# Kernel tuning notes

Hardware: AMD Instinct MI355X
Metric: run time of the kernel (lower is better)

The kernel has to match this reference:

```python
import jax, jax.numpy as jnp
import numpy as np

N = 50000
E = 600000
D_IN = 128
D_HID = 128
D_OUT = 40
EPS = 1e-5


def glorot(key, shape):
    lim = float(np.sqrt(6.0 / (shape[0] + shape[1])))
    return jax.random.uniform(key, shape, jnp.float32, -lim, lim)


def setup_inputs() -> dict:
    key = jax.random.key(0)
    ks = jax.random.split(key, 8)
    return {
        "node_feat": jax.random.normal(ks[0], (N, D_IN), jnp.float32),
        "edge_src": jax.random.randint(ks[1], (E,), 0, N, jnp.int32),
        "edge_dst": jax.random.randint(ks[2], (E,), 0, N, jnp.int32),
        # input BatchNorm (bn_1)
        "bn0_g": jnp.ones((D_IN,), jnp.float32),
        "bn0_b": jnp.zeros((D_IN,), jnp.float32),
        # conv 1 (in -> hidden) + its BN
        "W1": glorot(ks[3], (D_IN, D_HID)),
        "b1": jnp.zeros((D_HID,), jnp.float32),
        "bn1_g": jnp.ones((D_HID,), jnp.float32),
        "bn1_b": jnp.zeros((D_HID,), jnp.float32),
        # conv 2 (hidden -> hidden) + its BN
        "W2": glorot(ks[4], (D_HID, D_HID)),
        "b2": jnp.zeros((D_HID,), jnp.float32),
        "bn2_g": jnp.ones((D_HID,), jnp.float32),
        "bn2_b": jnp.zeros((D_HID,), jnp.float32),
        # final projection
        "Wf": glorot(ks[5], (D_HID, D_OUT)),
        "bf": jnp.zeros((D_OUT,), jnp.float32),
    }


def batchnorm(x, gamma, beta):
    # BatchNorm1d over nodes (batch-stat / training-mode normalization)
    mu = jnp.mean(x, axis=0)
    var = jnp.mean(jnp.square(x - mu), axis=0)
    return gamma * (x - mu) * jax.lax.rsqrt(var + EPS) + beta


def gcn_conv(x, W, b, src, dst, norm, self_norm):
    # GCNConv: D^{-1/2}(A+I)D^{-1/2} X W + b
    h = x @ W  # [N, d_out]
    agg = jax.ops.segment_sum(h[src] * norm[:, None], dst, num_segments=N)
    agg = agg + h * self_norm[:, None]  # self-loop contribution
    return agg + b


def reference(node_feat, edge_src, edge_dst, bn0_g, bn0_b, W1, b1, bn1_g, bn1_b,
              W2, b2, bn2_g, bn2_b, Wf, bf):
    # degree with self-loops: deg_i = |{e : dst(e)=i}| + 1
    deg = jnp.ones((N,), jnp.float32).at[edge_dst].add(1.0)
    dinv = jax.lax.rsqrt(deg)
    norm = dinv[edge_src] * dinv[edge_dst]  # [E]
    self_norm = dinv * dinv                 # [N]

    x = batchnorm(node_feat, bn0_g, bn0_b)

    x = gcn_conv(x, W1, b1, edge_src, edge_dst, norm, self_norm)
    x = batchnorm(x, bn1_g, bn1_b)
    x = jax.nn.relu(x)  # dropout is identity in eval mode

    x = gcn_conv(x, W2, b2, edge_src, edge_dst, norm, self_norm)
    x = batchnorm(x, bn2_g, bn2_b)
    x = jax.nn.relu(x)

    return x @ Wf + bf  # [N, D_OUT]
```

## Files before the change

kernel.cpp:

```cpp
#include <hip/hip_runtime.h>
#include <cstdint>
#include <cstddef>


#define CS_BLOCKS 512

typedef short s8v __attribute__((ext_vector_type(8)));
typedef float f4v __attribute__((ext_vector_type(4)));

__device__ inline ushort f2bf(float f) {
    uint u = __float_as_uint(f);
    return (ushort)((u + 0x7fffu + ((u >> 16) & 1u)) >> 16);
}
__device__ inline float2 bf2f2(uint u) {
    float2 r;
    r.x = __uint_as_float(u << 16);
    r.y = __uint_as_float(u & 0xffff0000u);
    return r;
}

__global__ __launch_bounds__(256) void k_prolog(const float* __restrict__ X,
                                                int n, float* __restrict__ part,
                                                const float* __restrict__ W1,
                                                const float* __restrict__ W2,
                                                ushort* __restrict__ Wswz,
                                                int* __restrict__ cnt) {
    const int bid = blockIdx.x;
    if (bid < CS_BLOCKS) {
        __shared__ float ls[8 * 128];
        __shared__ float lq[8 * 128];
        const int c4    = threadIdx.x & 31;
        const int rslot = threadIdx.x >> 5;
        float4 s4 = make_float4(0.f, 0.f, 0.f, 0.f);
        float4 q4 = make_float4(0.f, 0.f, 0.f, 0.f);
        const float4* X4 = (const float4*)X;
        for (int r = bid * 8 + rslot; r < n; r += CS_BLOCKS * 8) {
            float4 v = X4[(size_t)r * 32 + c4];
            s4.x += v.x; s4.y += v.y; s4.z += v.z; s4.w += v.w;
            q4.x = fmaf(v.x, v.x, q4.x); q4.y = fmaf(v.y, v.y, q4.y);
            q4.z = fmaf(v.z, v.z, q4.z); q4.w = fmaf(v.w, v.w, q4.w);
        }
        *(float4*)&ls[rslot * 128 + c4 * 4] = s4;
        *(float4*)&lq[rslot * 128 + c4 * 4] = q4;
        __syncthreads();
        float t = 0.f;
        if (threadIdx.x < 128) {
            int c = threadIdx.x;
            #pragma unroll
            for (int k = 0; k < 8; ++k) t += ls[k * 128 + c];
        } else {
            int c = threadIdx.x - 128;
            #pragma unroll
            for (int k = 0; k < 8; ++k) t += lq[k * 128 + c];
        }
        part[bid * 256 + threadIdx.x] = t;
    } else if (bid < CS_BLOCKS + 16) {
        const int wb = bid - CS_BLOCKS;
        const float* W = (wb < 8) ? W1 : W2;
        ushort* out = Wswz + (wb < 8 ? 0 : 16384);
        int t  = (wb & 7) * 256 + threadIdx.x;
        int l  = t & 63;
        int fi = t >> 6;
        int ks = fi & 3, ct = fi >> 2;
        int c  = ct * 16 + (l & 15);
        int k0 = ks * 32 + ((l >> 4) << 3);
        ushort o[8];
        #pragma unroll
        for (int j = 0; j < 8; ++j)
            o[j] = f2bf(W[(size_t)(k0 + j) * 128 + c]);
        ushort4* dst = (ushort4*)(out + (size_t)t * 8);
        dst[0] = make_ushort4(o[0], o[1], o[2], o[3]);
        dst[1] = make_ushort4(o[4], o[5], o[6], o[7]);
    } else {
        const int zb = bid - CS_BLOCKS - 16;
        const int nv = n >> 2;
        int4* c4p = (int4*)cnt;
        const int4 z = make_int4(0, 0, 0, 0);
        for (int i = zb * 256 + threadIdx.x; i < nv; i += 64 * 256)
            c4p[i] = z;
        int i = (nv << 2) + zb * 256 + threadIdx.x;
        if (i < n) cnt[i] = 0;
    }
}

__global__ __launch_bounds__(256) void k_redA(const float* __restrict__ part,
                                              float* __restrict__ part2,
                                              int nrows) {
    const int c = threadIdx.x;
    const int b = blockIdx.x;
    const int per = (nrows + 63) >> 6;
    const int r0 = b * per;
    const int r1 = min(r0 + per, nrows);
    float t0 = 0.f, t1 = 0.f;
    int r = r0;
    for (; r + 2 <= r1; r += 2) {
        t0 += part[(size_t)r * 256 + c];
        t1 += part[(size_t)(r + 1) * 256 + c];
    }
    if (r < r1) t0 += part[(size_t)r * 256 + c];
    part2[b * 256 + c] = t0 + t1;
}

__global__ __launch_bounds__(1024) void k_bnfinal(const float* __restrict__ part,
                                                  int nrows,
                                                  const float* __restrict__ g,
                                                  const float* __restrict__ be,
                                                  float invn,
                                                  float* __restrict__ a,
                                                  float* __restrict__ b) {
    __shared__ float sh[4][256];
    const int c = threadIdx.x & 255;
    const int q = threadIdx.x >> 8;
    const int per = nrows >> 2;
    float t = 0.f;
    for (int r = q * per; r < q * per + per; r += 4) {
        t += part[(r + 0) * 256 + c] + part[(r + 1) * 256 + c]
           + part[(r + 2) * 256 + c] + part[(r + 3) * 256 + c];
    }
    sh[q][c] = t;
    __syncthreads();
    if (threadIdx.x < 128) {
        int cc = threadIdx.x;
        float su = sh[0][cc] + sh[1][cc] + sh[2][cc] + sh[3][cc];
        float sq = sh[0][cc + 128] + sh[1][cc + 128]
                 + sh[2][cc + 128] + sh[3][cc + 128];
        float mu  = su * invn;
        float var = sq * invn - mu * mu;
        float av  = g[cc] * rsqrtf(var + 1e-5f);
        a[cc] = av;
        b[cc] = be[cc] - mu * av;
    }
}

__global__ __launch_bounds__(256) void k_count(const int* __restrict__ dst, int e,
                                               int* __restrict__ cnt,
                                               int* __restrict__ rank) {
    int i = blockIdx.x * 256 + threadIdx.x;
    if (i < e) rank[i] = atomicAdd(&cnt[dst[i]], 1);
}

__global__ __launch_bounds__(1024) void k_scanA(const int* __restrict__ cnt, int n,
                                                int* __restrict__ rs, int* __restrict__ bsum) {
    __shared__ int tmp[1024];
    int t = threadIdx.x;
    int i = blockIdx.x * 1024 + t;
    int v = (i < n) ? cnt[i] : 0;
    tmp[t] = v;
    __syncthreads();
    for (int off = 1; off < 1024; off <<= 1) {
        int x = (t >= off) ? tmp[t - off] : 0;
        __syncthreads();
        tmp[t] += x;
        __syncthreads();
    }
    if (i < n) rs[i] = tmp[t] - v;
    if (t == 1023) bsum[blockIdx.x] = tmp[t];
}

__global__ __launch_bounds__(256) void k_scanC(int* __restrict__ rs,
                                               const int* __restrict__ bsum,
                                               const int* __restrict__ cnt,
                                               float* __restrict__ dinv,
                                               int n, int e) {
    __shared__ int base;
    int chunk = (int)(blockIdx.x >> 2);
    if (threadIdx.x == 0) {
        int s = 0;
        for (int c = 0; c < chunk; ++c) s += bsum[c];
        base = s;
    }
    __syncthreads();
    int i = blockIdx.x * 256 + threadIdx.x;
    if (i < n) {
        rs[i] += base;
        dinv[i] = rsqrtf((float)(cnt[i] + 1));
    }
    if (blockIdx.x == 0 && threadIdx.x == 0) rs[n] = e;
}

__global__ __launch_bounds__(256) void k_fill(const int* __restrict__ src,
                                              const int* __restrict__ dst, int e,
                                              const int* __restrict__ rs,
                                              const int* __restrict__ rank,
                                              const float* __restrict__ dinv,
                                              int2* __restrict__ ep) {
    int i = blockIdx.x * 256 + threadIdx.x;
    if (i < e) {
        int d = dst[i], s = src[i];
        int p = rs[d] + rank[i];
        float nm = dinv[s] * dinv[d];
        ep[p] = make_int2(s, __float_as_int(nm));
    }
}

__global__ __launch_bounds__(256) void k_gemm_mfma(const float* __restrict__ X,
                                                   const ushort* __restrict__ Wswz,
                                                   const float* __restrict__ av,
                                                   const float* __restrict__ bv,
                                                   int relu,
                                                   ushort* __restrict__ H, int n) {
    __shared__ ushort xb[64 * 128];
    const int tid  = threadIdx.x;
    const int row0 = blockIdx.x * 64;

    for (int i = tid; i < 64 * 32; i += 256) {
        int r = i >> 5, c4 = i & 31;
        int gr = row0 + r;
        float4 v = make_float4(0.f, 0.f, 0.f, 0.f);
        if (gr < n) v = ((const float4*)X)[(size_t)gr * 32 + c4];
        float4 a4 = ((const float4*)av)[c4];
        float4 b4 = ((const float4*)bv)[c4];
        v.x = fmaf(v.x, a4.x, b4.x);
        v.y = fmaf(v.y, a4.y, b4.y);
        v.z = fmaf(v.z, a4.z, b4.z);
        v.w = fmaf(v.w, a4.w, b4.w);
        if (relu) {
            v.x = fmaxf(v.x, 0.f); v.y = fmaxf(v.y, 0.f);
            v.z = fmaxf(v.z, 0.f); v.w = fmaxf(v.w, 0.f);
        }
        ushort4 pk = make_ushort4(f2bf(v.x), f2bf(v.y), f2bf(v.z), f2bf(v.w));
        int off = (r * 256 + c4 * 8) ^ ((r & 7) << 4);
        *(ushort4*)((char*)xb + off) = pk;
    }
    __syncthreads();

    const int wv = tid >> 6;
    const int l  = tid & 63;
    const int arow = wv * 16 + (l & 15);

    s8v afr[4];
    #pragma unroll
    for (int ks = 0; ks < 4; ++ks) {
        int off = (arow * 256 + ks * 64 + ((l >> 4) << 4)) ^ ((arow & 7) << 4);
        afr[ks] = *(const s8v*)((const char*)xb + off);
    }

    const s8v* wf = (const s8v*)Wswz;
    f4v acc[8];
    #pragma unroll
    for (int ct = 0; ct < 8; ++ct) {
        f4v c = {0.f, 0.f, 0.f, 0.f};
        #pragma unroll
        for (int ks = 0; ks < 4; ++ks) {
            s8v bb = wf[(ct * 4 + ks) * 64 + l];
            c = __builtin_amdgcn_mfma_f32_16x16x32_bf16(afr[ks], bb, c, 0, 0, 0);
        }
        acc[ct] = c;
    }

    const int rbase = row0 + wv * 16 + ((l >> 4) << 2);
    const int cidx  = l & 15;
    #pragma unroll
    for (int r = 0; r < 4; ++r) {
        int gr = rbase + r;
        if (gr < n) {
            #pragma unroll
            for (int ct = 0; ct < 8; ++ct)
                H[(size_t)gr * 128 + ct * 16 + cidx] = f2bf(acc[ct][r]);
        }
    }
}

template<int NP>
__device__ inline void pair_batch(const ushort* __restrict__ H,
                                  const int2* __restrict__ ep,
                                  int i, int half, int sl,
                                  float& a0, float& a1, float& a2, float& a3) {
    int2 p[NP]; uint2 v[NP];
    #pragma unroll
    for (int k = 0; k < NP; ++k) p[k] = ep[i + 2 * k + half];
    #pragma unroll
    for (int k = 0; k < NP; ++k)
        v[k] = ((const uint2*)(H + (size_t)p[k].x * 128))[sl];
    #pragma unroll
    for (int k = 0; k < NP; ++k) {
        float w = __int_as_float(p[k].y);
        float2 f0 = bf2f2(v[k].x);
        float2 f1 = bf2f2(v[k].y);
        a0 = fmaf(w, f0.x, a0); a1 = fmaf(w, f0.y, a1);
        a2 = fmaf(w, f1.x, a2); a3 = fmaf(w, f1.y, a3);
    }
}

__global__ __launch_bounds__(256) void k_aggregate(const ushort* __restrict__ H,
                                                   const int* __restrict__ rs,
                                                   const int2* __restrict__ ep,
                                                   const float* __restrict__ dinv,
                                                   float* __restrict__ AGG,
                                                   float* __restrict__ part, int n) {
    __shared__ float red[4][128];
    __shared__ float redq[4][128];
    const int wv   = threadIdx.x >> 6;
    const int lane = threadIdx.x & 63;
    const int half = lane >> 5;
    const int sl   = lane & 31;
    const int node = blockIdx.x * 4 + wv;
    float a0 = 0.f, a1 = 0.f, a2 = 0.f, a3 = 0.f;

    if (node < n) {
        if (half == 0) {
            float sn = dinv[node]; sn *= sn;
            uint2 sv = ((const uint2*)(H + (size_t)node * 128))[sl];
            float2 f0 = bf2f2(sv.x), f1 = bf2f2(sv.y);
            a0 = sn * f0.x; a1 = sn * f0.y;
            a2 = sn * f1.x; a3 = sn * f1.y;
        }
        int i  = rs[node];
        int i1 = rs[node + 1];
        for (; i + 16 <= i1; i += 16) pair_batch<8>(H, ep, i, half, sl, a0, a1, a2, a3);
        if (i + 8 <= i1) { pair_batch<4>(H, ep, i, half, sl, a0, a1, a2, a3); i += 8; }
        if (i + 4 <= i1) { pair_batch<2>(H, ep, i, half, sl, a0, a1, a2, a3); i += 4; }
        if (i + 2 <= i1) { pair_batch<1>(H, ep, i, half, sl, a0, a1, a2, a3); i += 2; }
        if (i < i1) {
            int2 p = ep[i];
            float w = (half == 0) ? __int_as_float(p.y) : 0.f;
            uint2 v = ((const uint2*)(H + (size_t)p.x * 128))[sl];
            float2 f0 = bf2f2(v.x), f1 = bf2f2(v.y);
            a0 = fmaf(w, f0.x, a0); a1 = fmaf(w, f0.y, a1);
            a2 = fmaf(w, f1.x, a2); a3 = fmaf(w, f1.y, a3);
        }
        a0 += __shfl_xor(a0, 32);
        a1 += __shfl_xor(a1, 32);
        a2 += __shfl_xor(a2, 32);
        a3 += __shfl_xor(a3, 32);
        if (half == 0)
            ((float4*)(AGG + (size_t)node * 128))[sl] =
                make_float4(a0, a1, a2, a3);
    }

    if (half == 0) {
        *(float4*)&red[wv][4 * sl]  = make_float4(a0, a1, a2, a3);
        *(float4*)&redq[wv][4 * sl] = make_float4(a0 * a0, a1 * a1,
                                                  a2 * a2, a3 * a3);
    }
    __syncthreads();
    const int t = threadIdx.x;
    if (t < 128)
        part[(size_t)blockIdx.x * 256 + t] =
            red[0][t] + red[1][t] + red[2][t] + red[3][t];
    else {
        int c = t - 128;
        part[(size_t)blockIdx.x * 256 + t] =
            redq[0][c] + redq[1][c] + redq[2][c] + redq[3][c];
    }
}

__global__ __launch_bounds__(256) void k_gemm_out(const float* __restrict__ X,
                                                  const float* __restrict__ Wf,
                                                  const float* __restrict__ bfv,
                                                  const float* __restrict__ a,
                                                  const float* __restrict__ b,
                                                  float* __restrict__ OUT, int n) {
    __shared__ float xl[32 * 132];
    __shared__ float wt[40 * 132];
    const int tid = threadIdx.x;

    for (int i = tid; i < 128 * 40; i += 256) {
        int c = i / 40;
        int j = i - c * 40;
        wt[j * 132 + c] = Wf[i];
    }
    const int row0 = blockIdx.x * 32;
    for (int i = tid; i < 32 * 32; i += 256) {
        int r = i >> 5, c4 = i & 31;
        int gr = row0 + r;
        float4 v = make_float4(0.f, 0.f, 0.f, 0.f);
        if (gr < n) v = ((const float4*)X)[(size_t)gr * 32 + c4];
        float4 a4 = ((const float4*)a)[c4];
        float4 b4 = ((const float4*)b)[c4];
        v.x = fmaxf(fmaf(v.x, a4.x, b4.x), 0.f);
        v.y = fmaxf(fmaf(v.y, a4.y, b4.y), 0.f);
        v.z = fmaxf(fmaf(v.z, a4.z, b4.z), 0.f);
        v.w = fmaxf(fmaf(v.w, a4.w, b4.w), 0.f);
        *(float4*)&xl[r * 132 + (c4 << 2)] = v;
    }
    __syncthreads();

    const int rg = tid >> 3;
    const int cg = tid & 7;
    const int j0 = cg * 5;
    float acc[5] = {0.f, 0.f, 0.f, 0.f, 0.f};
    for (int c = 0; c < 128; c += 4) {
        float4 xv = *(const float4*)&xl[rg * 132 + c];
        #pragma unroll
        for (int j = 0; j < 5; ++j) {
            float4 wv = *(const float4*)&wt[(j0 + j) * 132 + c];
            acc[j] = fmaf(xv.x, wv.x, acc[j]);
            acc[j] = fmaf(xv.y, wv.y, acc[j]);
            acc[j] = fmaf(xv.z, wv.z, acc[j]);
            acc[j] = fmaf(xv.w, wv.w, acc[j]);
        }
    }
    int gr = row0 + rg;
    if (gr < n) {
        #pragma unroll
        for (int j = 0; j < 5; ++j)
            OUT[(size_t)gr * 40 + j0 + j] = acc[j] + bfv[j0 + j];
    }
}

extern "C" void kernel_launch(void* const* d_in, const int* in_sizes, int n_in,
                              void* d_out, int out_size, void* d_ws, size_t ws_size,
                              hipStream_t stream) {
    const float* X0      = (const float*)d_in[0];
    const int*   edgesrc = (const int*)d_in[1];
    const int*   edgedst = (const int*)d_in[2];
    const float* bn0g = (const float*)d_in[3];
    const float* bn0b = (const float*)d_in[4];
    const float* W1   = (const float*)d_in[5];
    const float* bn1g = (const float*)d_in[7];
    const float* bn1b = (const float*)d_in[8];
    const float* W2   = (const float*)d_in[9];
    const float* bn2g = (const float*)d_in[11];
    const float* bn2b = (const float*)d_in[12];
    const float* Wf   = (const float*)d_in[13];
    const float* bfv  = (const float*)d_in[14];

    const int n = in_sizes[0] / 128;
    const int e = in_sizes[1];
    float* OUT = (float*)d_out;

    const int aggBlocks = (n + 3) / 4;

    ushort* H    = (ushort*)d_ws;
    float*  AGG  = (float*)(H + (size_t)n * 128);
    float*  dinv = AGG + (size_t)n * 128;
    int2*   ep   = (int2*)(dinv + n);
    ushort* Wswz = (ushort*)(ep + e);
    int*    cnt  = (int*)(Wswz + 2 * 16384);
    int*    rs   = cnt + n;
    int*    rank = rs + n + 1;
    int*    bsum = rank + e;
    float*  part = (float*)(bsum + 64);
    float* part2 = part + (size_t)aggBlocks * 256;
    float* a0 = part2 + 64 * 256;       float* b0 = a0 + 128;
    float* a1 = b0 + 128;               float* b1 = a1 + 128;
    float* a2 = b1 + 128;               float* b2 = a2 + 128;

    const float invn = 1.f / (float)n;
    const int nb = (n + 1023) / 1024;

    k_prolog<<<CS_BLOCKS + 16 + 64, 256, 0, stream>>>(X0, n, part, W1, W2,
                                                      Wswz, cnt);

    k_count<<<(e + 255) / 256, 256, 0, stream>>>(edgedst, e, cnt, rank);
    k_scanA<<<nb, 1024, 0, stream>>>(cnt, n, rs, bsum);
    k_scanC<<<(n + 255) / 256, 256, 0, stream>>>(rs, bsum, cnt, dinv, n, e);
    k_fill<<<(e + 255) / 256, 256, 0, stream>>>(edgesrc, edgedst, e, rs, rank,
                                                dinv, ep);

    const int gemmBlocks = (n + 63) / 64;

    k_bnfinal<<<1, 1024, 0, stream>>>(part, CS_BLOCKS, bn0g, bn0b, invn, a0, b0);
    k_gemm_mfma<<<gemmBlocks, 256, 0, stream>>>(X0, Wswz, a0, b0, 0, H, n);
    k_aggregate<<<aggBlocks, 256, 0, stream>>>(H, rs, ep, dinv, AGG, part, n);

    k_redA<<<64, 256, 0, stream>>>(part, part2, aggBlocks);
    k_bnfinal<<<1, 1024, 0, stream>>>(part2, 64, bn1g, bn1b, invn, a1, b1);
    k_gemm_mfma<<<gemmBlocks, 256, 0, stream>>>(AGG, Wswz + 16384, a1, b1, 1, H, n);
    k_aggregate<<<aggBlocks, 256, 0, stream>>>(H, rs, ep, dinv, AGG, part, n);

    k_redA<<<64, 256, 0, stream>>>(part, part2, aggBlocks);
    k_bnfinal<<<1, 1024, 0, stream>>>(part2, 64, bn2g, bn2b, invn, a2, b2);
    k_gemm_out<<<(n + 31) / 32, 256, 0, stream>>>(AGG, Wf, bfv, a2, b2, OUT, n);
}
```

Measured before the change: 244.5 us.

## Fuse BN finalize into GEMM prologues and widen aggregate gathers to 16 bytes

Drops the single-block k_bnfinal launches. Each GEMM block now reduces the 64-row partial sums itself and computes the BN scale and shift in shared memory, which removes three serialized tiny kernels at the cost of redundant per-block reduction work. The aggregation kernel switches from two half-wave edge streams with 8-byte loads to four quarter-wave streams with 16-byte bf16 loads, combined by two shuffle stages. This raises memory-level parallelism per node for the gather.

```diff
diff --git a/kernel.cpp b/kernel.cpp
--- a/kernel.cpp
+++ b/kernel.cpp
@@ -101,35 +101,26 @@
     part2[b * 256 + c] = t0 + t1;
 }
 
-__global__ __launch_bounds__(1024) void k_bnfinal(const float* __restrict__ part,
-                                                  int nrows,
-                                                  const float* __restrict__ g,
-                                                  const float* __restrict__ be,
-                                                  float invn,
-                                                  float* __restrict__ a,
-                                                  float* __restrict__ b) {
-    __shared__ float sh[4][256];
-    const int c = threadIdx.x & 255;
-    const int q = threadIdx.x >> 8;
-    const int per = nrows >> 2;
+__device__ inline void bn_inblock(const float* __restrict__ part2,
+                                  const float* __restrict__ g,
+                                  const float* __restrict__ be,
+                                  float invn, float* __restrict__ tmp,
+                                  float* __restrict__ abuf,
+                                  float* __restrict__ bbuf) {
+    const int tid = threadIdx.x;
     float t = 0.f;
-    for (int r = q * per; r < q * per + per; r += 4) {
-        t += part[(r + 0) * 256 + c] + part[(r + 1) * 256 + c]
-           + part[(r + 2) * 256 + c] + part[(r + 3) * 256 + c];
-    }
-    sh[q][c] = t;
-    __syncthreads();
-    if (threadIdx.x < 128) {
-        int cc = threadIdx.x;
-        float su = sh[0][cc] + sh[1][cc] + sh[2][cc] + sh[3][cc];
-        float sq = sh[0][cc + 128] + sh[1][cc + 128]
-                 + sh[2][cc + 128] + sh[3][cc + 128];
-        float mu  = su * invn;
-        float var = sq * invn - mu * mu;
-        float av  = g[cc] * rsqrtf(var + 1e-5f);
-        a[cc] = av;
-        b[cc] = be[cc] - mu * av;
-    }
+    #pragma unroll 8
+    for (int r = 0; r < 64; ++r) t += part2[r * 256 + tid];
+    tmp[tid] = t;
+    __syncthreads();
+    if (tid < 128) {
+        float mu  = tmp[tid] * invn;
+        float var = tmp[tid + 128] * invn - mu * mu;
+        float av  = g[tid] * rsqrtf(var + 1e-5f);
+        abuf[tid] = av;
+        bbuf[tid] = be[tid] - mu * av;
+    }
+    __syncthreads();
 }
 
 __global__ __launch_bounds__(256) void k_count(const int* __restrict__ dst, int e,
@@ -195,21 +186,26 @@
 
 __global__ __launch_bounds__(256) void k_gemm_mfma(const float* __restrict__ X,
                                                    const ushort* __restrict__ Wswz,
-                                                   const float* __restrict__ av,
-                                                   const float* __restrict__ bv,
-                                                   int relu,
+                                                   const float* __restrict__ part2,
+                                                   const float* __restrict__ g,
+                                                   const float* __restrict__ be,
+                                                   float invn, int relu,
                                                    ushort* __restrict__ H, int n) {
     __shared__ ushort xb[64 * 128];
+    __shared__ float tmp[256];
+    __shared__ float abuf[128], bbuf[128];
     const int tid  = threadIdx.x;
     const int row0 = blockIdx.x * 64;
+
+    bn_inblock(part2, g, be, invn, tmp, abuf, bbuf);
 
     for (int i = tid; i < 64 * 32; i += 256) {
         int r = i >> 5, c4 = i & 31;
         int gr = row0 + r;
         float4 v = make_float4(0.f, 0.f, 0.f, 0.f);
         if (gr < n) v = ((const float4*)X)[(size_t)gr * 32 + c4];
-        float4 a4 = ((const float4*)av)[c4];
-        float4 b4 = ((const float4*)bv)[c4];
+        float4 a4 = *(const float4*)&abuf[c4 * 4];
+        float4 b4 = *(const float4*)&bbuf[c4 * 4];
         v.x = fmaf(v.x, a4.x, b4.x);
         v.y = fmaf(v.y, a4.y, b4.y);
         v.z = fmaf(v.z, a4.z, b4.z);
@@ -262,23 +258,24 @@
 }
 
 template<int NP>
-__device__ inline void pair_batch(const ushort* __restrict__ H,
+__device__ inline void quad_batch(const ushort* __restrict__ H,
                                   const int2* __restrict__ ep,
-                                  int i, int half, int sl,
-                                  float& a0, float& a1, float& a2, float& a3) {
-    int2 p[NP]; uint2 v[NP];
-    #pragma unroll
-    for (int k = 0; k < NP; ++k) p[k] = ep[i + 2 * k + half];
+                                  int i, int q, int sl, float* __restrict__ a) {
+    int2 p[NP]; uint4 v[NP];
+    #pragma unroll
+    for (int k = 0; k < NP; ++k) p[k] = ep[i + 4 * k + q];
     #pragma unroll
     for (int k = 0; k < NP; ++k)
-        v[k] = ((const uint2*)(H + (size_t)p[k].x * 128))[sl];
+        v[k] = ((const uint4*)(H + (size_t)p[k].x * 128))[sl];
     #pragma unroll
     for (int k = 0; k < NP; ++k) {
         float w = __int_as_float(p[k].y);
-        float2 f0 = bf2f2(v[k].x);
-        float2 f1 = bf2f2(v[k].y);
-        a0 = fmaf(w, f0.x, a0); a1 = fmaf(w, f0.y, a1);
-        a2 = fmaf(w, f1.x, a2); a3 = fmaf(w, f1.y, a3);
+        float2 f0 = bf2f2(v[k].x), f1 = bf2f2(v[k].y);
+        float2 f2 = bf2f2(v[k].z), f3 = bf2f2(v[k].w);
+        a[0] = fmaf(w, f0.x, a[0]); a[1] = fmaf(w, f0.y, a[1]);
+        a[2] = fmaf(w, f1.x, a[2]); a[3] = fmaf(w, f1.y, a[3]);
+        a[4] = fmaf(w, f2.x, a[4]); a[5] = fmaf(w, f2.y, a[5]);
+        a[6] = fmaf(w, f3.x, a[6]); a[7] = fmaf(w, f3.y, a[7]);
     }
 }
 
@@ -292,46 +289,65 @@
     __shared__ float redq[4][128];
     const int wv   = threadIdx.x >> 6;
     const int lane = threadIdx.x & 63;
-    const int half = lane >> 5;
-    const int sl   = lane & 31;
+    const int q    = lane >> 4;
+    const int sl   = lane & 15;
     const int node = blockIdx.x * 4 + wv;
-    float a0 = 0.f, a1 = 0.f, a2 = 0.f, a3 = 0.f;
+    float a[8] = {0.f, 0.f, 0.f, 0.f, 0.f, 0.f, 0.f, 0.f};
 
     if (node < n) {
-        if (half == 0) {
+        if (q == 0) {
             float sn = dinv[node]; sn *= sn;
-            uint2 sv = ((const uint2*)(H + (size_t)node * 128))[sl];
+            uint4 sv = ((const uint4*)(H + (size_t)node * 128))[sl];
             float2 f0 = bf2f2(sv.x), f1 = bf2f2(sv.y);
-            a0 = sn * f0.x; a1 = sn * f0.y;
-            a2 = sn * f1.x; a3 = sn * f1.y;
+            float2 f2 = bf2f2(sv.z), f3 = bf2f2(sv.w);
+            a[0] = sn * f0.x; a[1] = sn * f0.y;
+            a[2] = sn * f1.x; a[3] = sn * f1.y;
+            a[4] = sn * f2.x; a[5] = sn * f2.y;
+            a[6] = sn * f3.x; a[7] = sn * f3.y;
         }
         int i  = rs[node];
         int i1 = rs[node + 1];
-        for (; i + 16 <= i1; i += 16) pair_batch<8>(H, ep, i, half, sl, a0, a1, a2, a3);
-        if (i + 8 <= i1) { pair_batch<4>(H, ep, i, half, sl, a0, a1, a2, a3); i += 8; }
-        if (i + 4 <= i1) { pair_batch<2>(H, ep, i, half, sl, a0, a1, a2, a3); i += 4; }
-        if (i + 2 <= i1) { pair_batch<1>(H, ep, i, half, sl, a0, a1, a2, a3); i += 2; }
+        for (; i + 16 <= i1; i += 16) quad_batch<4>(H, ep, i, q, sl, a);
+        if (i + 8 <= i1) { quad_batch<2>(H, ep, i, q, sl, a); i += 8; }
+        if (i + 4 <= i1) { quad_batch<1>(H, ep, i, q, sl, a); i += 4; }
         if (i < i1) {
-            int2 p = ep[i];
-            float w = (half == 0) ? __int_as_float(p.y) : 0.f;
-            uint2 v = ((const uint2*)(H + (size_t)p.x * 128))[sl];
+            int idx = min(i + q, i1 - 1);
+            int2 p = ep[idx];
+            float w = (i + q < i1) ? __int_as_float(p.y) : 0.f;
+            uint4 v = ((const uint4*)(H + (size_t)p.x * 128))[sl];
             float2 f0 = bf2f2(v.x), f1 = bf2f2(v.y);
-            a0 = fmaf(w, f0.x, a0); a1 = fmaf(w, f0.y, a1);
-            a2 = fmaf(w, f1.x, a2); a3 = fmaf(w, f1.y, a3);
-        }
-        a0 += __shfl_xor(a0, 32);
-        a1 += __shfl_xor(a1, 32);
-        a2 += __shfl_xor(a2, 32);
-        a3 += __shfl_xor(a3, 32);
-        if (half == 0)
-            ((float4*)(AGG + (size_t)node * 128))[sl] =
-                make_float4(a0, a1, a2, a3);
-    }
-
-    if (half == 0) {
-        *(float4*)&red[wv][4 * sl]  = make_float4(a0, a1, a2, a3);
-        *(float4*)&redq[wv][4 * sl] = make_float4(a0 * a0, a1 * a1,
-                                                  a2 * a2, a3 * a3);
+            float2 f2 = bf2f2(v.z), f3 = bf2f2(v.w);
+            a[0] = fmaf(w, f0.x, a[0]); a[1] = fmaf(w, f0.y, a[1]);
+            a[2] = fmaf(w, f1.x, a[2]); a[3] = fmaf(w, f1.y, a[3]);
+            a[4] = fmaf(w, f2.x, a[4]); a[5] = fmaf(w, f2.y, a[5]);
+            a[6] = fmaf(w, f3.x, a[6]); a[7] = fmaf(w, f3.y, a[7]);
+        }
+        #pragma unroll
+        for (int j = 0; j < 8; ++j) {
+            a[j] += __shfl_xor(a[j], 16);
+            a[j] += __shfl_xor(a[j], 32);
+        }
+        if (q == 0) {
+            float4* dst = (float4*)(AGG + (size_t)node * 128);
+            dst[2 * sl]     = make_float4(a[0], a[1], a[2], a[3]);
+            dst[2 * sl + 1] = make_float4(a[4], a[5], a[6], a[7]);
+        }
+    }
+
+    if (q == 0) {
+        *(float4*)&red[wv][8 * sl]      = make_float4(a[0], a[1], a[2], a[3]);
+        *(float4*)&red[wv][8 * sl + 4]  = make_float4(a[4], a[5], a[6], a[7]);
+        *(float4*)&redq[wv][8 * sl]     = make_float4(a[0] * a[0], a[1] * a[1],
+                                                      a[2] * a[2], a[3] * a[3]);
+        *(float4*)&redq[wv][8 * sl + 4] = make_float4(a[4] * a[4], a[5] * a[5],
+                                                      a[6] * a[6], a[7] * a[7]);
+    } else if (node >= n) {
+    }
+    if (q == 0 && node >= n) {
+        *(float4*)&red[wv][8 * sl]      = make_float4(0.f, 0.f, 0.f, 0.f);
+        *(float4*)&red[wv][8 * sl + 4]  = make_float4(0.f, 0.f, 0.f, 0.f);
+        *(float4*)&redq[wv][8 * sl]     = make_float4(0.f, 0.f, 0.f, 0.f);
+        *(float4*)&redq[wv][8 * sl + 4] = make_float4(0.f, 0.f, 0.f, 0.f);
     }
     __syncthreads();
     const int t = threadIdx.x;
@@ -348,12 +364,18 @@
 __global__ __launch_bounds__(256) void k_gemm_out(const float* __restrict__ X,
                                                   const float* __restrict__ Wf,
                                                   const float* __restrict__ bfv,
-                                                  const float* __restrict__ a,
-                                                  const float* __restrict__ b,
+                                                  const float* __restrict__ part2,
+                                                  const float* __restrict__ g,
+                                                  const float* __restrict__ be,
+                                                  float invn,
                                                   float* __restrict__ OUT, int n) {
     __shared__ float xl[32 * 132];
     __shared__ float wt[40 * 132];
+    __shared__ float tmp[256];
+    __shared__ float abuf[128], bbuf[128];
     const int tid = threadIdx.x;
+
+    bn_inblock(part2, g, be, invn, tmp, abuf, bbuf);
 
     for (int i = tid; i < 128 * 40; i += 256) {
         int c = i / 40;
@@ -366,8 +388,8 @@
         int gr = row0 + r;
         float4 v = make_float4(0.f, 0.f, 0.f, 0.f);
         if (gr < n) v = ((const float4*)X)[(size_t)gr * 32 + c4];
-        float4 a4 = ((const float4*)a)[c4];
-        float4 b4 = ((const float4*)b)[c4];
+        float4 a4 = *(const float4*)&abuf[c4 * 4];
+        float4 b4 = *(const float4*)&bbuf[c4 * 4];
         v.x = fmaxf(fmaf(v.x, a4.x, b4.x), 0.f);
         v.y = fmaxf(fmaf(v.y, a4.y, b4.y), 0.f);
         v.z = fmaxf(fmaf(v.z, a4.z, b4.z), 0.f);
@@ -433,9 +455,6 @@
     int*    bsum = rank + e;
     float*  part = (float*)(bsum + 64);
     float* part2 = part + (size_t)aggBlocks * 256;
-    float* a0 = part2 + 64 * 256;       float* b0 = a0 + 128;
-    float* a1 = b0 + 128;               float* b1 = a1 + 128;
-    float* a2 = b1 + 128;               float* b2 = a2 + 128;
 
     const float invn = 1.f / (float)n;
     const int nb = (n + 1023) / 1024;
@@ -451,16 +470,17 @@
 
     const int gemmBlocks = (n + 63) / 64;
 
-    k_bnfinal<<<1, 1024, 0, stream>>>(part, CS_BLOCKS, bn0g, bn0b, invn, a0, b0);
-    k_gemm_mfma<<<gemmBlocks, 256, 0, stream>>>(X0, Wswz, a0, b0, 0, H, n);
+    k_redA<<<64, 256, 0, stream>>>(part, part2, CS_BLOCKS);
+    k_gemm_mfma<<<gemmBlocks, 256, 0, stream>>>(X0, Wswz, part2, bn0g, bn0b,
+                                                invn, 0, H, n);
     k_aggregate<<<aggBlocks, 256, 0, stream>>>(H, rs, ep, dinv, AGG, part, n);
 
     k_redA<<<64, 256, 0, stream>>>(part, part2, aggBlocks);
-    k_bnfinal<<<1, 1024, 0, stream>>>(part2, 64, bn1g, bn1b, invn, a1, b1);
-    k_gemm_mfma<<<gemmBlocks, 256, 0, stream>>>(AGG, Wswz + 16384, a1, b1, 1, H, n);
+    k_gemm_mfma<<<gemmBlocks, 256, 0, stream>>>(AGG, Wswz + 16384, part2, bn1g,
+                                                bn1b, invn, 1, H, n);
     k_aggregate<<<aggBlocks, 256, 0, stream>>>(H, rs, ep, dinv, AGG, part, n);
 
     k_redA<<<64, 256, 0, stream>>>(part, part2, aggBlocks);
-    k_bnfinal<<<1, 1024, 0, stream>>>(part2, 64, bn2g, bn2b, invn, a2, b2);
-    k_gemm_out<<<(n + 31) / 32, 256, 0, stream>>>(AGG, Wf, bfv, a2, b2, OUT, n);
-}
+    k_gemm_out<<<(n + 31) / 32, 256, 0, stream>>>(AGG, Wf, bfv, part2, bn2g,
+                                                  bn2b, invn, OUT, n);
+}
```

New measurement: 239.7 us. 2.0% less time.
